# Kernel tuning notes

Measured on AMD Instinct MI355X. Metric: run time of the kernel, lower is better.

## Reference

```python
import jax, jax.numpy as jnp
import numpy as np

K = 5            # spline kernel size per dim
NUM_CLASSES = 10
EPS = 1e-4       # matches module's normalize eps
ROUTING_ITERS = 3
_BITS = jnp.array([[(b >> 2) & 1, (b >> 1) & 1, b & 1] for b in range(8)], dtype=jnp.float32)  # [8,3]


def normalize(t, axis=-1):
    return t / (jnp.sqrt(jnp.sum(t * t, axis=axis, keepdims=True)) + EPS)


def quat_mul(q, r):
    # quaternions stored (x, y, z, w) -- module sets identity as [:,:,:,3]=1
    qx, qy, qz, qw = q[..., 0], q[..., 1], q[..., 2], q[..., 3]
    rx, ry, rz, rw = r[..., 0], r[..., 1], r[..., 2], r[..., 3]
    return jnp.stack([
        qw * rx + qx * rw + qy * rz - qz * ry,
        qw * ry - qx * rz + qy * rw + qz * rx,
        qw * rz + qx * ry - qy * rx + qz * rw,
        qw * rw - qx * rx - qy * ry - qz * rz,
    ], axis=-1)


def spline_conv(x, pseudo, src, dst, W, root, bias, n_nodes):
    # degree-1 open B-spline conv, kernel 5^3, in=1, out=16
    v = pseudo * (K - 1)                                   # [E,3]
    i0 = jnp.clip(jnp.floor(v), 0, K - 2)                  # [E,3]
    frac = v - i0
    i0 = i0.astype(jnp.int32)
    idx = i0[:, None, :] + _BITS.astype(jnp.int32)[None]   # [E,8,3]
    kflat = (idx[..., 0] * K + idx[..., 1]) * K + idx[..., 2]  # [E,8]
    wb = jnp.prod(jnp.where(_BITS[None] > 0, frac[:, None, :], 1.0 - frac[:, None, :]), axis=-1)  # [E,8]
    Wg = W[kflat]                                          # [E,8,16] irregular gather (dominant traffic)
    wk = jnp.einsum('eb,ebo->eo', wb, Wg)                  # [E,16]
    msg = x[src] * wk                                      # [E,16] (in-channels = 1)
    agg = jax.ops.segment_sum(msg, dst, num_segments=n_nodes)
    deg = jax.ops.segment_sum(jnp.ones_like(dst, dtype=x.dtype), dst, num_segments=n_nodes)
    return agg / jnp.maximum(deg, 1.0)[:, None] + x @ root + bias


def caps_layer(pose, act, q):
    # pose [N,I,4], act [N,I], q [I,J,4] -> pose [N,J,4], act [N,J]
    qn = normalize(q)
    pred = normalize(quat_mul(qn[None], pose[:, :, None, :]))  # [N,I,J,4]
    b = jnp.zeros(pred.shape[:3], dtype=pose.dtype)
    for _ in range(ROUTING_ITERS):
        c = jax.nn.softmax(b, axis=2) * act[:, :, None]
        s = jnp.einsum('nij,nijq->njq', c, pred)
        v = normalize(s)
        b = b + jnp.einsum('nijq,njq->nij', pred, v)
    act_out = jax.nn.sigmoid(jnp.einsum('nij,nijq,njq->nj', c, pred, v))
    return v, act_out


def pool_by_agreement(pose, act, pos, G, start, size):
    # voxel-grid clustering + agreement-weighted quaternion averaging
    g = jnp.clip(jnp.floor((pos - start) / size), 0, G - 1).astype(jnp.int32)  # [N,3]
    vid = (g[:, 0] * G + g[:, 1]) * G + g[:, 2]
    V = G ** 3
    s = jax.ops.segment_sum(act[:, :, None] * pose, vid, num_segments=V)  # [V,J,4]
    m = normalize(s)
    agree = jnp.sum(pose * m[vid], axis=-1)                                # [N,J]
    wsum = jax.ops.segment_sum(act, vid, num_segments=V)
    cnt = jax.ops.segment_sum(jnp.ones((pose.shape[0],), pose.dtype), vid, num_segments=V)
    act_out = jax.nn.sigmoid(jax.ops.segment_sum(act * agree, vid, num_segments=V) / (wsum + EPS))
    pos_out = jax.ops.segment_sum(pos, vid, num_segments=V) / (cnt[:, None] + EPS)
    return m, act_out, pos_out


def forward(x, pos, pseudo, W_spline, root, bias, lin_w, lin_b, q0, q1, q3, q5, q6, q7, edge_index):
    N = x.shape[0]
    src, dst = edge_index[0], edge_index[1]
    h = spline_conv(x, pseudo, src, dst, W_spline, root, bias, N)   # [N,16]
    quats = jax.nn.elu(h) @ lin_w + lin_b                           # [N,4]
    pose = normalize(quats.reshape(N, 1, 4))                        # [N,1,4]
    act = x.reshape(N, 1)                                           # expand to num_caps_in=1
    pose, act = caps_layer(pose, act, q0)                           # 1 -> 6
    pose, act = caps_layer(pose, act, q1)                           # 6 -> 6
    min_pos, max_pos = pos.min(), pos.max()
    rng = max_pos + 0.001 - min_pos
    pose, act, p = pool_by_agreement(pose, act, pos, 32, min_pos, rng / 32)   # -> 32768 voxels
    pose, act = caps_layer(pose, act, q3)                           # 6 -> 8
    pose, act, p = pool_by_agreement(pose, act, p, 8, min_pos, rng / 8)       # -> 512
    pose, act = caps_layer(pose, act, q5)                           # 8 -> 12
    pose, act, p = pool_by_agreement(pose, act, p, 2, min_pos, rng / 2)       # -> 8
    pose, act = caps_layer(pose, act, q6)                           # 12 -> 14
    pose, act, p = pool_by_agreement(pose, act, p, 1, min_pos - 0.5, max_pos - min_pos + 1.0)  # -> 1
    pose, act = caps_layer(pose, act, q7)                           # 14 -> 10
    return act                                                      # [1, 10]


def setup_inputs() -> dict:
    key = jax.random.key(0)
    ks = jax.random.split(key, 16)
    N, E = 50000, 800000
    def caps_q(k, i, j):
        return jax.random.normal(k, (i, j, 4), dtype=jnp.float32)
    return {
        'x': jax.random.uniform(ks[0], (N, 1), dtype=jnp.float32),
        'pos': jax.random.uniform(ks[1], (N, 3), dtype=jnp.float32),
        'pseudo': jax.random.uniform(ks[2], (E, 3), dtype=jnp.float32),
        'W_spline': jax.random.normal(ks[3], (K ** 3, 16), dtype=jnp.float32) * 0.1,
        'root': jax.random.normal(ks[4], (1, 16), dtype=jnp.float32) * 0.1,
        'bias': jnp.zeros((16,), dtype=jnp.float32),
        'lin_w': jax.random.normal(ks[5], (16, 4), dtype=jnp.float32) * 0.25,
        'lin_b': jnp.zeros((4,), dtype=jnp.float32),
        'q0': caps_q(ks[6], 1, 6),
        'q1': caps_q(ks[7], 6, 6),
        'q3': caps_q(ks[8], 6, 8),
        'q5': caps_q(ks[9], 8, 12),
        'q6': caps_q(ks[10], 12, 14),
        'q7': caps_q(ks[11], 14, NUM_CLASSES),
        'edge_index': jax.random.randint(ks[12], (2, E), 0, N, dtype=jnp.int32),
    }


def reference(x, pos, pseudo, W_spline, root, bias, lin_w, lin_b, q0, q1, q3, q5, q6, q7, edge_index):
    return forward(x, pos, pseudo, W_spline, root, bias, lin_w, lin_b, q0, q1, q3, q5, q6, q7, edge_index)
```

## Files before the change

### kernel.cpp

```cpp
#include <hip/hip_runtime.h>
#include <math.h>

#define EPS 1e-4f

__device__ __forceinline__ float sigmoidf_(float x){ return 1.0f/(1.0f+expf(-x)); }

__device__ __forceinline__ unsigned f2u_(float f){
    unsigned u = __float_as_uint(f);
    return (u & 0x80000000u) ? ~u : (u | 0x80000000u);
}
__device__ __forceinline__ float u2f_(unsigned u){
    unsigned b = (u & 0x80000000u) ? (u & 0x7FFFFFFFu) : ~u;
    return __uint_as_float(b);
}

__global__ void minmax_kernel(const float* __restrict__ p, int n, unsigned* mm){
    float lo = INFINITY, hi = -INFINITY;
    for (int i = blockIdx.x*blockDim.x + threadIdx.x; i < n; i += gridDim.x*blockDim.x){
        float v = p[i]; lo = fminf(lo, v); hi = fmaxf(hi, v);
    }
    for (int off = 32; off > 0; off >>= 1){
        lo = fminf(lo, __shfl_down(lo, off));
        hi = fmaxf(hi, __shfl_down(hi, off));
    }
    __shared__ float slo[8], shi[8];
    int wid = threadIdx.x >> 6;
    if ((threadIdx.x & 63) == 0){ slo[wid] = lo; shi[wid] = hi; }
    __syncthreads();
    if (threadIdx.x == 0){
        int nw = blockDim.x >> 6;
        for (int w = 1; w < nw; w++){ lo = fminf(lo, slo[w]); hi = fmaxf(hi, shi[w]); }
        atomicMin(&mm[0], f2u_(lo));
        atomicMax(&mm[1], f2u_(hi));
    }
}

__global__ void elist_edge(const int* __restrict__ ei, int* __restrict__ head,
                           int* __restrict__ nxt, int E){
    int e = blockIdx.x*blockDim.x + threadIdx.x;
    if (e >= E) return;
    int d = ei[E + e];
    nxt[e] = atomicExch(&head[d], e);
}

__device__ __forceinline__ int voxel_id(const float* __restrict__ pos, int n, int G,
                                        float start, float size){
    int g[3];
    #pragma unroll
    for (int k = 0; k < 3; k++){
        float gg = floorf((pos[(size_t)n*3 + k] - start) / size);
        gg = fminf(fmaxf(gg, 0.f), (float)(G - 1));
        g[k] = (int)gg;
    }
    return (g[0]*G + g[1])*G + g[2];
}

__device__ __forceinline__ void pool_geom(const unsigned* mm, int G, int mode,
                                          float& start, float& size){
    float mn = u2f_(mm[0]), mx = u2f_(mm[1]);
    if (mode == 0){ start = mn; size = (mx + 0.001f - mn) / (float)G; }
    else          { start = mn - 0.5f; size = mx - mn + 1.0f; }
}

__global__ void elist_node(const float* __restrict__ pos, int* __restrict__ head,
                           int* __restrict__ nxt, int N, int G, int mode,
                           const unsigned* __restrict__ mm){
    int n = blockIdx.x*blockDim.x + threadIdx.x;
    if (n >= N) return;
    float start, size; pool_geom(mm, G, mode, start, size);
    int v = voxel_id(pos, n, G, start, size);
    nxt[n] = atomicExch(&head[v], n);
}

__global__ __launch_bounds__(64)
void spline_node_kernel(const float* __restrict__ x, const float* __restrict__ pseudo,
                        const int* __restrict__ ei,
                        const int* __restrict__ head, const int* __restrict__ nxt,
                        const float* __restrict__ W,
                        const float* __restrict__ root, const float* __restrict__ bias,
                        const float* __restrict__ lin_w, const float* __restrict__ lin_b,
                        float* __restrict__ pose, float* __restrict__ act, int N, int E){
    __shared__ float Ws[125*17];
    for (int i = threadIdx.x; i < 125*16; i += blockDim.x)
        Ws[(i >> 4)*17 + (i & 15)] = W[i];
    __syncthreads();
    int n = blockIdx.x*blockDim.x + threadIdx.x;
    if (n >= N) return;

    float agg[16];
    #pragma unroll
    for (int o = 0; o < 16; o++) agg[o] = 0.f;

    int cnt = 0;
    for (int e = head[n]; e >= 0; e = nxt[e]){
        float p0 = pseudo[3*e], p1 = pseudo[3*e+1], p2 = pseudo[3*e+2];
        int src = ei[e];
        float xv = x[src];
        float v0 = p0*4.f, v1 = p1*4.f, v2 = p2*4.f;
        float f0 = fminf(fmaxf(floorf(v0), 0.f), 3.f);
        float f1 = fminf(fmaxf(floorf(v1), 0.f), 3.f);
        float f2 = fminf(fmaxf(floorf(v2), 0.f), 3.f);
        float fr0 = v0 - f0, fr1 = v1 - f1, fr2 = v2 - f2;
        int i0 = (int)f0, i1 = (int)f1, i2 = (int)f2;
        #pragma unroll
        for (int b = 0; b < 8; b++){
            int b0 = (b >> 2) & 1, b1 = (b >> 1) & 1, b2 = b & 1;
            float w = (b0 ? fr0 : 1.f - fr0) * (b1 ? fr1 : 1.f - fr1) * (b2 ? fr2 : 1.f - fr2);
            w *= xv;
            int k = ((i0 + b0)*5 + (i1 + b1))*5 + (i2 + b2);
            const float* Wr = &Ws[k*17];
            #pragma unroll
            for (int o = 0; o < 16; o++) agg[o] += w * Wr[o];
        }
        cnt++;
    }

    float deg = fmaxf((float)cnt, 1.0f);
    float xs = x[n];
    float qv0 = lin_b[0], qv1 = lin_b[1], qv2 = lin_b[2], qv3 = lin_b[3];
    #pragma unroll
    for (int o = 0; o < 16; o++){
        float h = agg[o] / deg + xs * root[o] + bias[o];
        float e = (h > 0.f) ? h : expm1f(h);
        qv0 += e * lin_w[o*4 + 0];
        qv1 += e * lin_w[o*4 + 1];
        qv2 += e * lin_w[o*4 + 2];
        qv3 += e * lin_w[o*4 + 3];
    }
    float inv = 1.0f / (sqrtf(qv0*qv0 + qv1*qv1 + qv2*qv2 + qv3*qv3) + EPS);
    pose[(size_t)n*4 + 0] = qv0*inv;
    pose[(size_t)n*4 + 1] = qv1*inv;
    pose[(size_t)n*4 + 2] = qv2*inv;
    pose[(size_t)n*4 + 3] = qv3*inv;
    act[n] = xs;
}

template<int I, int J, int NPB>
__global__ __launch_bounds__(NPB*I*J)
void caps_coop_kernel(const float* __restrict__ poseIn, const float* __restrict__ actIn,
                      const float* __restrict__ q, float* __restrict__ poseOut,
                      float* __restrict__ actOut, int N){
    const int IJ = I*J;
    const int tid = threadIdx.x;
    const int nl  = tid / IJ;
    const int li  = tid - nl*IJ;
    const int i   = li / J;
    const int j   = li - i*J;
    const int node = blockIdx.x*NPB + nl;
    const bool on = (node < N);

    __shared__ float redA[NPB][I*J];
    __shared__ float redB[NPB][I*J];
    __shared__ float cp[NPB][I*J*4];
    __shared__ float vsh[NPB][J*4];

    float prx=0.f, pry=0.f, prz=0.f, prw=0.f, ai=0.f;
    if (on){
        float qx = q[li*4+0], qy = q[li*4+1], qz = q[li*4+2], qw = q[li*4+3];
        float qinv = 1.0f/(sqrtf(qx*qx+qy*qy+qz*qz+qw*qw)+EPS);
        qx*=qinv; qy*=qinv; qz*=qinv; qw*=qinv;
        const float* pp = &poseIn[((size_t)node*I + i)*4];
        float rx=pp[0], ry=pp[1], rz=pp[2], rw=pp[3];
        ai = actIn[(size_t)node*I + i];
        float tx = qw*rx + qx*rw + qy*rz - qz*ry;
        float ty = qw*ry - qx*rz + qy*rw + qz*rx;
        float tz = qw*rz + qx*ry - qy*rx + qz*rw;
        float tw = qw*rw - qx*rx - qy*ry - qz*rz;
        float pinv = 1.0f/(sqrtf(tx*tx+ty*ty+tz*tz+tw*tw)+EPS);
        prx=tx*pinv; pry=ty*pinv; prz=tz*pinv; prw=tw*pinv;
    }

    float b = 0.f, c = 0.f;
    for (int t = 0; t < 3; t++){
        redA[nl][li] = b;
        __syncthreads();
        float mb = -INFINITY;
        #pragma unroll
        for (int jj = 0; jj < J; jj++) mb = fmaxf(mb, redA[nl][i*J+jj]);
        float e = expf(b - mb);
        redB[nl][li] = e;
        __syncthreads();
        float s = 0.f;
        #pragma unroll
        for (int jj = 0; jj < J; jj++) s += redB[nl][i*J+jj];
        c = ai * e / s;
        cp[nl][li*4+0] = c*prx; cp[nl][li*4+1] = c*pry;
        cp[nl][li*4+2] = c*prz; cp[nl][li*4+3] = c*prw;
        __syncthreads();
        for (int idx = li; idx < J*4; idx += IJ){
            int jj = idx >> 2, comp = idx & 3;
            float acc = 0.f;
            #pragma unroll
            for (int ii = 0; ii < I; ii++) acc += cp[nl][(ii*J+jj)*4+comp];
            vsh[nl][idx] = acc;
        }
        __syncthreads();
        if (li < J){
            float a0=vsh[nl][li*4], a1=vsh[nl][li*4+1], a2=vsh[nl][li*4+2], a3=vsh[nl][li*4+3];
            float inv = 1.0f/(sqrtf(a0*a0+a1*a1+a2*a2+a3*a3)+EPS);
            vsh[nl][li*4]=a0*inv; vsh[nl][li*4+1]=a1*inv;
            vsh[nl][li*4+2]=a2*inv; vsh[nl][li*4+3]=a3*inv;
        }
        __syncthreads();
        if (t < 2){
            b += prx*vsh[nl][j*4] + pry*vsh[nl][j*4+1] + prz*vsh[nl][j*4+2] + prw*vsh[nl][j*4+3];
            __syncthreads();
        } else {
            redA[nl][li] = c*(prx*vsh[nl][j*4] + pry*vsh[nl][j*4+1]
                            + prz*vsh[nl][j*4+2] + prw*vsh[nl][j*4+3]);
            __syncthreads();
            if (li < J && on){
                float acc = 0.f;
                #pragma unroll
                for (int ii = 0; ii < I; ii++) acc += redA[nl][ii*J+li];
                actOut[(size_t)node*J + li] = sigmoidf_(acc);
                poseOut[((size_t)node*J+li)*4+0] = vsh[nl][li*4+0];
                poseOut[((size_t)node*J+li)*4+1] = vsh[nl][li*4+1];
                poseOut[((size_t)node*J+li)*4+2] = vsh[nl][li*4+2];
                poseOut[((size_t)node*J+li)*4+3] = vsh[nl][li*4+3];
            }
        }
    }
}

template<int J>
__global__ __launch_bounds__(256)
void pool1_gather_kernel(const float* __restrict__ pose, const float* __restrict__ act,
                         const float* __restrict__ pos,
                         const int* __restrict__ head, const int* __restrict__ nxt,
                         float* __restrict__ poseOut, float* __restrict__ actOut,
                         float* __restrict__ posOut, int V){
    int v = blockIdx.x*blockDim.x + threadIdx.x;
    if (v >= V) return;

    float s[J][4], w[J], ps0=0.f, ps1=0.f, ps2=0.f;
    #pragma unroll
    for (int j = 0; j < J; j++){ s[j][0]=0.f; s[j][1]=0.f; s[j][2]=0.f; s[j][3]=0.f; w[j]=0.f; }

    int cnt = 0;
    for (int n = head[v]; n >= 0; n = nxt[n]){
        const float* pb = &pose[(size_t)n*J*4];
        const float* ab = &act[(size_t)n*J];
        #pragma unroll
        for (int j = 0; j < J; j++){
            float aj = ab[j];
            s[j][0] += aj*pb[j*4+0];
            s[j][1] += aj*pb[j*4+1];
            s[j][2] += aj*pb[j*4+2];
            s[j][3] += aj*pb[j*4+3];
            w[j] += aj;
        }
        ps0 += pos[(size_t)n*3+0];
        ps1 += pos[(size_t)n*3+1];
        ps2 += pos[(size_t)n*3+2];
        cnt++;
    }
    #pragma unroll
    for (int j = 0; j < J; j++){
        float inv = 1.0f/(sqrtf(s[j][0]*s[j][0]+s[j][1]*s[j][1]+
                                s[j][2]*s[j][2]+s[j][3]*s[j][3])+EPS);
        s[j][0]*=inv; s[j][1]*=inv; s[j][2]*=inv; s[j][3]*=inv;
    }
    float ag[J];
    #pragma unroll
    for (int j = 0; j < J; j++) ag[j] = 0.f;
    for (int n = head[v]; n >= 0; n = nxt[n]){
        const float* pb = &pose[(size_t)n*J*4];
        const float* ab = &act[(size_t)n*J];
        #pragma unroll
        for (int j = 0; j < J; j++){
            float agree = pb[j*4+0]*s[j][0] + pb[j*4+1]*s[j][1]
                        + pb[j*4+2]*s[j][2] + pb[j*4+3]*s[j][3];
            ag[j] += ab[j]*agree;
        }
    }
    #pragma unroll
    for (int j = 0; j < J; j++){
        size_t o = (size_t)v*J + j;
        actOut[o] = sigmoidf_(ag[j] / (w[j] + EPS));
        poseOut[o*4+0] = s[j][0];
        poseOut[o*4+1] = s[j][1];
        poseOut[o*4+2] = s[j][2];
        poseOut[o*4+3] = s[j][3];
    }
    float c = (float)cnt + EPS;
    posOut[(size_t)v*3+0] = ps0 / c;
    posOut[(size_t)v*3+1] = ps1 / c;
    posOut[(size_t)v*3+2] = ps2 / c;
}

template<int V, int J, int CH, int NCHUNK>
__global__ void pool_priv1(const float4* __restrict__ poseIn, const float* __restrict__ actIn,
                           const float* __restrict__ posIn,
                           float* __restrict__ s, float* __restrict__ wsum,
                           float* __restrict__ cnt, float* __restrict__ psum,
                           int N, int G, int mode, const unsigned* __restrict__ mm){
    __shared__ float s_[V*CH*4];
    __shared__ float wsum_[V*CH];
    __shared__ float cnt_[V];
    __shared__ float psum_[V*3];
    const int chunk = blockIdx.x % NCHUNK;
    const int slice = blockIdx.x / NCHUNK;
    const int nslices = gridDim.x / NCHUNK;
    const int c0 = chunk * CH;

    for (int t = threadIdx.x; t < V*CH*4; t += blockDim.x) s_[t] = 0.f;
    for (int t = threadIdx.x; t < V*CH; t += blockDim.x) wsum_[t] = 0.f;
    if (chunk == 0){
        for (int t = threadIdx.x; t < V; t += blockDim.x) cnt_[t] = 0.f;
        for (int t = threadIdx.x; t < V*3; t += blockDim.x) psum_[t] = 0.f;
    }
    __syncthreads();

    float start, size; pool_geom(mm, G, mode, start, size);
    int per = (N + nslices - 1) / nslices;
    int n0 = slice * per, n1 = min(N, n0 + per);

    for (int n = n0 + (int)threadIdx.x; n < n1; n += blockDim.x){
        int vid = voxel_id(posIn, n, G, start, size);
        #pragma unroll
        for (int jj = 0; jj < CH; jj++){
            int j = c0 + jj;
            float aj = actIn[(size_t)n*J + j];
            float4 p = poseIn[(size_t)n*J + j];
            int b = (vid*CH + jj)*4;
            atomicAdd(&s_[b+0], aj*p.x);
            atomicAdd(&s_[b+1], aj*p.y);
            atomicAdd(&s_[b+2], aj*p.z);
            atomicAdd(&s_[b+3], aj*p.w);
            atomicAdd(&wsum_[vid*CH + jj], aj);
        }
        if (chunk == 0){
            atomicAdd(&cnt_[vid], 1.0f);
            atomicAdd(&psum_[vid*3+0], posIn[(size_t)n*3+0]);
            atomicAdd(&psum_[vid*3+1], posIn[(size_t)n*3+1]);
            atomicAdd(&psum_[vid*3+2], posIn[(size_t)n*3+2]);
        }
    }
    __syncthreads();

    for (int t = threadIdx.x; t < V*CH*4; t += blockDim.x){
        float val = s_[t];
        if (val != 0.f){
            int v = t / (CH*4), r = t % (CH*4);
            atomicAdd(&s[((size_t)v*J + c0)*4 + r], val);
        }
    }
    for (int t = threadIdx.x; t < V*CH; t += blockDim.x){
        float val = wsum_[t];
        if (val != 0.f){
            int v = t / CH, jj = t % CH;
            atomicAdd(&wsum[(size_t)v*J + c0 + jj], val);
        }
    }
    if (chunk == 0){
        for (int t = threadIdx.x; t < V; t += blockDim.x)
            if (cnt_[t] != 0.f) atomicAdd(&cnt[t], cnt_[t]);
        for (int t = threadIdx.x; t < V*3; t += blockDim.x)
            if (psum_[t] != 0.f) atomicAdd(&psum[t], psum_[t]);
    }
}

template<int V, int J>
__global__ void pool_priv2(const float4* __restrict__ poseIn, const float* __restrict__ actIn,
                           const float* __restrict__ posIn, const float4* __restrict__ m,
                           float* __restrict__ agacc,
                           int N, int G, int mode, const unsigned* __restrict__ mm){
    __shared__ float ag_[V*J];
    for (int t = threadIdx.x; t < V*J; t += blockDim.x) ag_[t] = 0.f;
    __syncthreads();
    float start, size; pool_geom(mm, G, mode, start, size);
    int nslices = gridDim.x;
    int per = (N + nslices - 1) / nslices;
    int n0 = blockIdx.x * per, n1 = min(N, n0 + per);
    for (int n = n0 + (int)threadIdx.x; n < n1; n += blockDim.x){
        int vid = voxel_id(posIn, n, G, start, size);
        #pragma unroll
        for (int j = 0; j < J; j++){
            float4 p  = poseIn[(size_t)n*J + j];
            float4 mv = m[(size_t)vid*J + j];
            float agree = p.x*mv.x + p.y*mv.y + p.z*mv.z + p.w*mv.w;
            atomicAdd(&ag_[vid*J + j], actIn[(size_t)n*J + j]*agree);
        }
    }
    __syncthreads();
    for (int t = threadIdx.x; t < V*J; t += blockDim.x)
        if (ag_[t] != 0.f) atomicAdd(&agacc[t], ag_[t]);
}

__global__ void pool_m(const float* __restrict__ s, float* __restrict__ m, int VJ){
    int t = blockIdx.x*blockDim.x + threadIdx.x;
    if (t >= VJ) return;
    float a = s[(size_t)t*4], b = s[(size_t)t*4+1], c = s[(size_t)t*4+2], d = s[(size_t)t*4+3];
    float inv = 1.0f / (sqrtf(a*a + b*b + c*c + d*d) + EPS);
    m[(size_t)t*4]   = a*inv;
    m[(size_t)t*4+1] = b*inv;
    m[(size_t)t*4+2] = c*inv;
    m[(size_t)t*4+3] = d*inv;
}

__global__ void pool_fin(const float* __restrict__ agacc, const float* __restrict__ wsum,
                         const float* __restrict__ cnt, const float* __restrict__ psum,
                         float* __restrict__ actOut, float* __restrict__ posOut, int V, int J){
    int t = blockIdx.x*blockDim.x + threadIdx.x;
    if (t >= V*J) return;
    int v = t / J, j = t % J;
    actOut[t] = sigmoidf_(agacc[t] / (wsum[t] + EPS));
    if (j == 0){
        float c = cnt[v] + EPS;
        posOut[(size_t)v*3 + 0] = psum[(size_t)v*3 + 0] / c;
        posOut[(size_t)v*3 + 1] = psum[(size_t)v*3 + 1] / c;
        posOut[(size_t)v*3 + 2] = psum[(size_t)v*3 + 2] / c;
    }
}

template<int V, int J, int CH>
__global__ void pool_fused_kernel(const float* __restrict__ poseIn, const float* __restrict__ actIn,
                                  const float* __restrict__ posIn,
                                  float* __restrict__ poseOut, float* __restrict__ actOut,
                                  float* __restrict__ posOut,
                                  int N, int G, int mode, const unsigned* __restrict__ mm){
    __shared__ float s_[V*CH*4];
    __shared__ float wsum_[V*CH];
    __shared__ float ag_[V*CH];
    __shared__ float cnt_[V];
    __shared__ float psum_[V*3];
    const int c0 = blockIdx.x * CH;

    for (int t = threadIdx.x; t < V*CH*4; t += blockDim.x) s_[t] = 0.f;
    for (int t = threadIdx.x; t < V*CH; t += blockDim.x){ wsum_[t] = 0.f; ag_[t] = 0.f; }
    if (blockIdx.x == 0){
        for (int t = threadIdx.x; t < V; t += blockDim.x) cnt_[t] = 0.f;
        for (int t = threadIdx.x; t < V*3; t += blockDim.x) psum_[t] = 0.f;
    }
    __syncthreads();

    float start, size; pool_geom(mm, G, mode, start, size);

    for (int n = threadIdx.x; n < N; n += blockDim.x){
        int vid = voxel_id(posIn, n, G, start, size);
        #pragma unroll
        for (int jj = 0; jj < CH; jj++){
            int j = c0 + jj;
            float aj = actIn[(size_t)n*J + j];
            const float* pb = &poseIn[((size_t)n*J + j)*4];
            int b = (vid*CH + jj)*4;
            atomicAdd(&s_[b+0], aj*pb[0]);
            atomicAdd(&s_[b+1], aj*pb[1]);
            atomicAdd(&s_[b+2], aj*pb[2]);
            atomicAdd(&s_[b+3], aj*pb[3]);
            atomicAdd(&wsum_[vid*CH + jj], aj);
        }
        if (blockIdx.x == 0){
            atomicAdd(&cnt_[vid], 1.0f);
            atomicAdd(&psum_[vid*3+0], posIn[(size_t)n*3+0]);
            atomicAdd(&psum_[vid*3+1], posIn[(size_t)n*3+1]);
            atomicAdd(&psum_[vid*3+2], posIn[(size_t)n*3+2]);
        }
    }
    __syncthreads();

    for (int t = threadIdx.x; t < V*CH; t += blockDim.x){
        float a = s_[t*4], b = s_[t*4+1], c = s_[t*4+2], d = s_[t*4+3];
        float inv = 1.0f / (sqrtf(a*a + b*b + c*c + d*d) + EPS);
        s_[t*4] = a*inv; s_[t*4+1] = b*inv; s_[t*4+2] = c*inv; s_[t*4+3] = d*inv;
    }
    __syncthreads();

    for (int n = threadIdx.x; n < N; n += blockDim.x){
        int vid = voxel_id(posIn, n, G, start, size);
        #pragma unroll
        for (int jj = 0; jj < CH; jj++){
            int j = c0 + jj;
            const float* pb = &poseIn[((size_t)n*J + j)*4];
            const float* mb = &s_[(vid*CH + jj)*4];
            float agree = pb[0]*mb[0] + pb[1]*mb[1] + pb[2]*mb[2] + pb[3]*mb[3];
            atomicAdd(&ag_[vid*CH + jj], actIn[(size_t)n*J + j]*agree);
        }
    }
    __syncthreads();

    for (int t = threadIdx.x; t < V*CH; t += blockDim.x){
        int v = t / CH, jj = t % CH;
        size_t o = (size_t)v*J + c0 + jj;
        actOut[o] = sigmoidf_(ag_[t] / (wsum_[t] + EPS));
        poseOut[o*4+0] = s_[t*4+0];
        poseOut[o*4+1] = s_[t*4+1];
        poseOut[o*4+2] = s_[t*4+2];
        poseOut[o*4+3] = s_[t*4+3];
    }
    if (blockIdx.x == 0){
        for (int v = threadIdx.x; v < V; v += blockDim.x){
            float c = cnt_[v] + EPS;
            posOut[(size_t)v*3+0] = psum_[(size_t)v*3+0] / c;
            posOut[(size_t)v*3+1] = psum_[(size_t)v*3+1] / c;
            posOut[(size_t)v*3+2] = psum_[(size_t)v*3+2] / c;
        }
    }
}

extern "C" void kernel_launch(void* const* d_in, const int* in_sizes, int n_in,
                              void* d_out, int out_size, void* d_ws, size_t ws_size,
                              hipStream_t stream){
    const float* x      = (const float*)d_in[0];
    const float* pos    = (const float*)d_in[1];
    const float* pseudo = (const float*)d_in[2];
    const float* Wsp    = (const float*)d_in[3];
    const float* root   = (const float*)d_in[4];
    const float* bias   = (const float*)d_in[5];
    const float* lin_w  = (const float*)d_in[6];
    const float* lin_b  = (const float*)d_in[7];
    const float* q0     = (const float*)d_in[8];
    const float* q1     = (const float*)d_in[9];
    const float* q3     = (const float*)d_in[10];
    const float* q5     = (const float*)d_in[11];
    const float* q6     = (const float*)d_in[12];
    const float* q7     = (const float*)d_in[13];
    const int*   ei     = (const int*)d_in[14];
    const int N = in_sizes[0];
    const int E = in_sizes[2] / 3;
    const int V1 = 32768;

    char* ws = (char*)d_ws;
    size_t off = 0;
    auto alloc = [&](size_t bytes)->void*{
        void* p = ws + off;
        off += (bytes + 255) & ~(size_t)255;
        return p;
    };
    unsigned* mm   = (unsigned*)alloc(8);
    int* ehead     = (int*)alloc((size_t)N*sizeof(int));
    int* enxt      = (int*)alloc((size_t)E*sizeof(int));
    int* vhead     = (int*)alloc((size_t)V1*sizeof(int));
    int* vnxt      = (int*)alloc((size_t)N*sizeof(int));
    float* P0  = (float*)alloc((size_t)1250000*sizeof(float));
    float* P1  = (float*)alloc((size_t)1250000*sizeof(float));
    float* A0  = (float*)alloc((size_t)310000*sizeof(float));
    float* A1  = (float*)alloc((size_t)310000*sizeof(float));
    float* PB0 = (float*)alloc((size_t)100000*sizeof(float));
    float* PB1 = (float*)alloc((size_t)100000*sizeof(float));
    size_t pool_off0 = off;
    float* vs  = (float*)alloc((size_t)512*8*4*sizeof(float));
    float* vw  = (float*)alloc((size_t)512*8*sizeof(float));
    float* va  = (float*)alloc((size_t)512*8*sizeof(float));
    float* vc  = (float*)alloc((size_t)512*sizeof(float));
    float* vp  = (float*)alloc((size_t)512*3*sizeof(float));
    size_t pool_bytes = off - pool_off0;

    hipMemsetAsync(mm,     0xFF, 4, stream);
    hipMemsetAsync(mm + 1, 0x00, 4, stream);
    hipMemsetAsync(ehead, 0xFF, (size_t)N*sizeof(int), stream);
    hipMemsetAsync(vhead, 0xFF, (size_t)V1*sizeof(int), stream);

    minmax_kernel<<<80, 256, 0, stream>>>(pos, N*3, mm);

    elist_edge<<<(E + 255)/256, 256, 0, stream>>>(ei, ehead, enxt, E);
    spline_node_kernel<<<(N + 63)/64, 64, 0, stream>>>(x, pseudo, ei, ehead, enxt, Wsp,
                                                       root, bias, lin_w, lin_b, P0, A0, N, E);

    caps_coop_kernel<1,6,32><<<(N + 31)/32, 32*6, 0, stream>>>(P0, A0, q0, P1, A1, N);
    caps_coop_kernel<6,6,7><<<(N + 6)/7, 7*36, 0, stream>>>(P1, A1, q1, P0, A0, N);

    {
        const int G = 32;
        elist_node<<<(N + 255)/256, 256, 0, stream>>>(pos, vhead, vnxt, N, G, 0, mm);
        pool1_gather_kernel<6><<<(V1 + 255)/256, 256, 0, stream>>>(P0, A0, pos, vhead, vnxt,
                                                                   P1, A1, PB0, V1);
    }
    caps_coop_kernel<6,8,5><<<(32768 + 4)/5, 5*48, 0, stream>>>(P1, A1, q3, P0, A0, 32768);

    {
        const int V = 512, J = 8, G = 8, NSL = 64;
        hipMemsetAsync(vs, 0, pool_bytes, stream);
        pool_priv1<V,J,4,2><<<2*NSL, 256, 0, stream>>>((const float4*)P0, A0, PB0,
                                                       vs, vw, vc, vp, 32768, G, 0, mm);
        pool_m<<<(V*J + 255)/256, 256, 0, stream>>>(vs, P1, V*J);
        pool_priv2<V,J><<<NSL, 256, 0, stream>>>((const float4*)P0, A0, PB0,
                                                 (const float4*)P1, va, 32768, G, 0, mm);
        pool_fin<<<(V*J + 255)/256, 256, 0, stream>>>(va, vw, vc, vp, A1, PB1, V, J);
    }
    caps_coop_kernel<8,12,2><<<256, 2*96, 0, stream>>>(P1, A1, q5, P0, A0, 512);

    {
        const int V = 8, J = 12, G = 2, NSL = 16;
        hipMemsetAsync(vs, 0, pool_bytes, stream);
        pool_priv1<V,J,12,1><<<NSL, 256, 0, stream>>>((const float4*)P0, A0, PB1,
                                                      vs, vw, vc, vp, 512, G, 0, mm);
        pool_m<<<1, 256, 0, stream>>>(vs, P1, V*J);
        pool_priv2<V,J><<<NSL, 256, 0, stream>>>((const float4*)P0, A0, PB1,
                                                 (const float4*)P1, va, 512, G, 0, mm);
        pool_fin<<<1, 256, 0, stream>>>(va, vw, vc, vp, A1, PB0, V, J);
    }
    caps_coop_kernel<12,14,1><<<8, 168, 0, stream>>>(P1, A1, q6, P0, A0, 8);

    pool_fused_kernel<1,14,14><<<1, 1024, 0, stream>>>(P0, A0, PB0, P1, A1, PB1, 8, 1, 1, mm);
    caps_coop_kernel<14,10,1><<<1, 140, 0, stream>>>(P1, A1, q7, P0, (float*)d_out, 1);
}
```

Baseline: 339.1 us.

## Split per-node edge lists into four sublists processed by four lanes

Edges are spread across four linked-list heads per destination node (chosen by edge index mod 4), and the spline kernel assigns four lanes per node. Each lane walks one shorter chain, and the partial sums are combined with xor shuffles. This is meant to cut the serial pointer-chasing latency per node and raise parallelism. In exchange it quadruples the head array and its memset, and the block size grows to 256.

```diff
diff --git a/kernel.cpp b/kernel.cpp
--- a/kernel.cpp
+++ b/kernel.cpp
@@ -36,11 +36,11 @@
 }
 
 __global__ void elist_edge(const int* __restrict__ ei, int* __restrict__ head,
-                           int* __restrict__ nxt, int E){
+                           int* __restrict__ nxt, int E, int N){
     int e = blockIdx.x*blockDim.x + threadIdx.x;
     if (e >= E) return;
     int d = ei[E + e];
-    nxt[e] = atomicExch(&head[d], e);
+    nxt[e] = atomicExch(&head[(e & 3)*N + d], e);
 }
 
 __device__ __forceinline__ int voxel_id(const float* __restrict__ pos, int n, int G,
@@ -72,7 +72,7 @@
     nxt[n] = atomicExch(&head[v], n);
 }
 
-__global__ __launch_bounds__(64)
+__global__ __launch_bounds__(256)
 void spline_node_kernel(const float* __restrict__ x, const float* __restrict__ pseudo,
                         const int* __restrict__ ei,
                         const int* __restrict__ head, const int* __restrict__ nxt,
@@ -84,7 +84,9 @@
     for (int i = threadIdx.x; i < 125*16; i += blockDim.x)
         Ws[(i >> 4)*17 + (i & 15)] = W[i];
     __syncthreads();
-    int n = blockIdx.x*blockDim.x + threadIdx.x;
+    int t = blockIdx.x*blockDim.x + threadIdx.x;
+    int n = t >> 2;
+    int k = t & 3;
     if (n >= N) return;
 
     float agg[16];
@@ -92,10 +94,9 @@
     for (int o = 0; o < 16; o++) agg[o] = 0.f;
 
     int cnt = 0;
-    for (int e = head[n]; e >= 0; e = nxt[e]){
+    for (int e = head[k*N + n]; e >= 0; e = nxt[e]){
         float p0 = pseudo[3*e], p1 = pseudo[3*e+1], p2 = pseudo[3*e+2];
-        int src = ei[e];
-        float xv = x[src];
+        float xv = x[ei[e]];
         float v0 = p0*4.f, v1 = p1*4.f, v2 = p2*4.f;
         float f0 = fminf(fmaxf(floorf(v0), 0.f), 3.f);
         float f1 = fminf(fmaxf(floorf(v1), 0.f), 3.f);
@@ -107,13 +108,23 @@
             int b0 = (b >> 2) & 1, b1 = (b >> 1) & 1, b2 = b & 1;
             float w = (b0 ? fr0 : 1.f - fr0) * (b1 ? fr1 : 1.f - fr1) * (b2 ? fr2 : 1.f - fr2);
             w *= xv;
-            int k = ((i0 + b0)*5 + (i1 + b1))*5 + (i2 + b2);
-            const float* Wr = &Ws[k*17];
+            int kk = ((i0 + b0)*5 + (i1 + b1))*5 + (i2 + b2);
+            const float* Wr = &Ws[kk*17];
             #pragma unroll
             for (int o = 0; o < 16; o++) agg[o] += w * Wr[o];
         }
         cnt++;
     }
+
+    #pragma unroll
+    for (int o = 0; o < 16; o++){
+        agg[o] += __shfl_xor(agg[o], 1);
+        agg[o] += __shfl_xor(agg[o], 2);
+    }
+    cnt += __shfl_xor(cnt, 1);
+    cnt += __shfl_xor(cnt, 2);
+
+    if (k != 0) return;
 
     float deg = fmaxf((float)cnt, 1.0f);
     float xs = x[n];
@@ -529,7 +540,7 @@
         return p;
     };
     unsigned* mm   = (unsigned*)alloc(8);
-    int* ehead     = (int*)alloc((size_t)N*sizeof(int));
+    int* ehead     = (int*)alloc((size_t)4*N*sizeof(int));
     int* enxt      = (int*)alloc((size_t)E*sizeof(int));
     int* vhead     = (int*)alloc((size_t)V1*sizeof(int));
     int* vnxt      = (int*)alloc((size_t)N*sizeof(int));
@@ -549,14 +560,14 @@
 
     hipMemsetAsync(mm,     0xFF, 4, stream);
     hipMemsetAsync(mm + 1, 0x00, 4, stream);
-    hipMemsetAsync(ehead, 0xFF, (size_t)N*sizeof(int), stream);
+    hipMemsetAsync(ehead, 0xFF, (size_t)4*N*sizeof(int), stream);
     hipMemsetAsync(vhead, 0xFF, (size_t)V1*sizeof(int), stream);
 
     minmax_kernel<<<80, 256, 0, stream>>>(pos, N*3, mm);
 
-    elist_edge<<<(E + 255)/256, 256, 0, stream>>>(ei, ehead, enxt, E);
-    spline_node_kernel<<<(N + 63)/64, 64, 0, stream>>>(x, pseudo, ei, ehead, enxt, Wsp,
-                                                       root, bias, lin_w, lin_b, P0, A0, N, E);
+    elist_edge<<<(E + 255)/256, 256, 0, stream>>>(ei, ehead, enxt, E, N);
+    spline_node_kernel<<<(4*N + 255)/256, 256, 0, stream>>>(x, pseudo, ei, ehead, enxt, Wsp,
+                                                            root, bias, lin_w, lin_b, P0, A0, N, E);
 
     caps_coop_kernel<1,6,32><<<(N + 31)/32, 32*6, 0, stream>>>(P0, A0, q0, P1, A1, N);
     caps_coop_kernel<6,6,7><<<(N + 6)/7, 7*36, 0, stream>>>(P1, A1, q1, P0, A0, N);
```

New measurement: 334.5 us. About the same (-1.4%).
